# Optimization experiments

Measured on AMD Instinct MI355X. Metric: run time of the kernel, lower is better.

Reference implementation:

```python
import jax, jax.numpy as jnp
import numpy as np

N = 50000      # nodes
E = 800000     # edges (avg degree 16)
NODE = 64      # node_attr_size
EDGE = 16      # edge_attr_size
H = 2          # gat_heads
C = 64         # hidden_size (per-head out channels)
F = H * C      # feature_size = 128
L = 2          # num_gat_layers
K = 10         # num_clusters
EPS = 1e-5
NEG_SLOPE = 0.2


def setup_inputs() -> dict:
    key = jax.random.key(0)
    ks = jax.random.split(key, 16)
    s = 0.05
    inp = {
        "x": jax.random.normal(ks[0], (N, NODE), jnp.float32),
        "edge_index": jax.random.randint(ks[1], (2, E), 0, N, jnp.int64 if jax.config.read('jax_enable_x64') else jnp.int32),
        "edge_attr": jax.random.normal(ks[2], (E, EDGE), jnp.float32),
        # node_feat_proj
        "Wp": jax.random.normal(ks[3], (NODE, F), jnp.float32) * s,
        "bp": jnp.zeros((F,), jnp.float32),
        # per-layer LayerNorm affine params, stacked over layers
        "ln_g": jnp.ones((L, F), jnp.float32),
        "ln_b": jnp.zeros((L, F), jnp.float32),
        # per-layer GATv2Conv params (PyG: lin_l, lin_r with bias, lin_edge no bias, att, out bias)
        "Wl": jax.random.normal(ks[4], (L, F, F), jnp.float32) * s,
        "bl": jnp.zeros((L, F), jnp.float32),
        "Wr": jax.random.normal(ks[5], (L, F, F), jnp.float32) * s,
        "br": jnp.zeros((L, F), jnp.float32),
        "We": jax.random.normal(ks[6], (L, EDGE, F), jnp.float32) * s,
        "att": jax.random.normal(ks[7], (L, H, C), jnp.float32) * s,
        "bout": jnp.zeros((L, F), jnp.float32),
        # classifier
        "Wc": jax.random.normal(ks[8], (F, K), jnp.float32) * s,
        "bc": jnp.zeros((K,), jnp.float32),
    }
    return inp


def _layer_norm(x, g, b):
    mu = jnp.mean(x, axis=-1, keepdims=True)
    var = jnp.var(x, axis=-1, keepdims=True)
    return (x - mu) * jax.lax.rsqrt(var + EPS) * g + b


def _gatv2_conv(x, src, dst, Wl, bl, Wr, br, We, att, bout):
    # x: [N, F] -> out: [N, H*C]
    xl = (x @ Wl + bl).reshape(N, H, C)          # source transform
    xr = (x @ Wr + br).reshape(N, H, C)          # target transform
    ee = (jnp.zeros(0),)  # placeholder, edge emb computed by caller closure
    return xl, xr


def reference(x, edge_index, edge_attr, Wp, bp, ln_g, ln_b, Wl, bl, Wr, br, We, att, bout, Wc, bc):
    src, dst = edge_index[0], edge_index[1]
    h = x @ Wp + bp                                   # [N, F]
    for i in range(L):
        identity = h
        hn = _layer_norm(h, ln_g[i], ln_b[i])
        xl = (hn @ Wl[i] + bl[i]).reshape(N, H, C)    # lin_l(x)  (source side)
        xr = (hn @ Wr[i] + br[i]).reshape(N, H, C)    # lin_r(x)  (target side)
        ee = (edge_attr @ We[i]).reshape(E, H, C)     # lin_edge(edge_attr)
        m = xl[src] + xr[dst] + ee                    # [E, H, C]
        m = jnp.where(m > 0, m, NEG_SLOPE * m)        # LeakyReLU(0.2)
        logits = jnp.einsum('ehc,hc->eh', m, att[i])  # [E, H]
        # segment softmax over incoming edges of each target node
        mx = jax.ops.segment_max(logits, dst, num_segments=N)
        ex = jnp.exp(logits - mx[dst])
        den = jax.ops.segment_sum(ex, dst, num_segments=N)
        alpha = ex / den[dst]                         # [E, H]
        msg = xl[src] * alpha[:, :, None]             # [E, H, C]
        agg = jax.ops.segment_sum(msg, dst, num_segments=N)  # [N, H, C]
        hg = agg.reshape(N, F) + bout[i]
        h = jax.nn.relu(hg) + identity                # relu -> dropout(eval no-op) -> residual add
    node_embeddings = h
    classification_output = h @ Wc + bc               # [N, K]
    return (classification_output, node_embeddings)
```

## Files before the change

kernel.cpp:

```cpp
#include <hip/hip_runtime.h>
#include <math.h>

#define N_NODES 50000
#define N_EDGES 800000
#define FDIM 128
#define KCLS 10

typedef float v2f __attribute__((ext_vector_type(2)));
typedef short bf16x8 __attribute__((ext_vector_type(8)));
typedef float f32x4 __attribute__((ext_vector_type(4)));

__device__ __forceinline__ v2f pksplat(float a) { v2f r; r.x = a; r.y = a; return r; }
__device__ __forceinline__ v2f pkfma(v2f a, v2f b, v2f c) { return __builtin_elementwise_fma(a, b, c); }
__device__ __forceinline__ v2f pklrelu(v2f v) {
    v2f z = pksplat(0.f);
    v2f mx = __builtin_elementwise_max(v, z);
    v2f mn = __builtin_elementwise_min(v, z);
    return pkfma(pksplat(0.2f), mn, mx);
}
__device__ __forceinline__ int rfl(int v) { return __builtin_amdgcn_readfirstlane(v); }

__device__ __forceinline__ unsigned int f2bfu(float f) {
    unsigned int u = __float_as_uint(f);
    u += 0x7FFFu + ((u >> 16) & 1u);
    return u >> 16;
}

__device__ __forceinline__ float half_sum32(float x) {
    int v;
    v = __builtin_amdgcn_update_dpp(0, __float_as_int(x), 0xB1, 0xF, 0xF, true);
    x += __int_as_float(v);
    v = __builtin_amdgcn_update_dpp(0, __float_as_int(x), 0x4E, 0xF, 0xF, true);
    x += __int_as_float(v);
    v = __builtin_amdgcn_update_dpp(0, __float_as_int(x), 0x124, 0xF, 0xF, true);
    x += __int_as_float(v);
    v = __builtin_amdgcn_update_dpp(0, __float_as_int(x), 0x128, 0xF, 0xF, true);
    x += __int_as_float(v);
    v = __builtin_amdgcn_ds_swizzle(__float_as_int(x), 0x401F);
    x += __int_as_float(v);
    return x;
}


__global__ void k_count(const int* __restrict__ dst, int* __restrict__ indeg, int e_total) {
    int e = blockIdx.x * 256 + threadIdx.x;
    if (e < e_total) atomicAdd(&indeg[dst[e]], 1);
}

__global__ __launch_bounds__(1024) void k_scan_block(const int* __restrict__ in, int* __restrict__ excl,
                                                     int* __restrict__ bsum, int n) {
    __shared__ int sh[1024];
    int t = threadIdx.x;
    int g = blockIdx.x * 1024 + t;
    int v = (g < n) ? in[g] : 0;
    sh[t] = v;
    __syncthreads();
    for (int d = 1; d < 1024; d <<= 1) {
        int x = (t >= d) ? sh[t - d] : 0;
        __syncthreads();
        sh[t] += x;
        __syncthreads();
    }
    if (g < n) excl[g] = sh[t] - v;
    if (t == 1023) bsum[blockIdx.x] = sh[t];
}

__global__ void k_scan_small(int* bsum, int nb) {
    if (threadIdx.x == 0 && blockIdx.x == 0) {
        int run = 0;
        for (int i = 0; i < nb; i++) { int v = bsum[i]; bsum[i] = run; run += v; }
    }
}

__global__ __launch_bounds__(1024) void k_scan_add(int* __restrict__ offs, const int* __restrict__ bsum,
                                                   int* __restrict__ cursor, int n, int e_total) {
    int g = blockIdx.x * 1024 + threadIdx.x;
    if (g < n) {
        int v = offs[g] + bsum[blockIdx.x];
        offs[g] = v;
        cursor[g] = v;
    }
    if (g == 0) offs[n] = e_total;
}

__global__ void k_scatter_fused(const int* __restrict__ src, const int* __restrict__ dst,
                                const float* __restrict__ edge_attr,
                                int* __restrict__ cursor, int* __restrict__ ssrc,
                                float* __restrict__ sea, int e_total) {
    int e = blockIdx.x * 256 + threadIdx.x;
    if (e < e_total) {
        int d = dst[e];
        int p = atomicAdd(&cursor[d], 1);
        ssrc[p] = src[e];
        const float4* ea = (const float4*)&edge_attr[(size_t)e * 16];
        float4* out = (float4*)&sea[(size_t)p * 16];
        float4 a = ea[0], b = ea[1], c = ea[2], q = ea[3];
        out[0] = a; out[1] = b; out[2] = c; out[3] = q;
    }
}

__global__ void k_scatter(const int* __restrict__ src, const int* __restrict__ dst,
                          int* __restrict__ cursor, int* __restrict__ seid, int* __restrict__ ssrc, int e_total) {
    int e = blockIdx.x * 256 + threadIdx.x;
    if (e < e_total) {
        int d = dst[e];
        int p = atomicAdd(&cursor[d], 1);
        seid[p] = e;
        ssrc[p] = src[e];
    }
}


__global__ void k_prep_w(const float* __restrict__ Wp, const float* __restrict__ Wl,
                         const float* __restrict__ Wr,
                         short* __restrict__ Wpt, short* __restrict__ Wlt, short* __restrict__ Wrt) {
    int i = blockIdx.x * 256 + threadIdx.x;
    if (i < 128 * 64) {
        int nn = i >> 6, k = i & 63;
        Wpt[i] = (short)f2bfu(Wp[k * 128 + nn]);
    }
    if (i < 2 * 128 * 128) {
        int L = i >> 14, r = i & 16383;
        int nn = r >> 7, k = r & 127;
        Wlt[i] = (short)f2bfu(Wl[L * 16384 + k * 128 + nn]);
        Wrt[i] = (short)f2bfu(Wr[L * 16384 + k * 128 + nn]);
    }
}


__device__ __forceinline__ void ln_to_shn_bf16(float a0[4][4], const float* __restrict__ lng,
                                               const float* __restrict__ lnb, short* __restrict__ shn,
                                               int tr, int tc) {
    float4 g4 = *(const float4*)&lng[tc];
    float4 b4 = *(const float4*)&lnb[tc];
#pragma unroll
    for (int j = 0; j < 4; j++) {
        float s = (a0[j][0] + a0[j][1]) + (a0[j][2] + a0[j][3]);
        float ss = a0[j][0] * a0[j][0] + a0[j][1] * a0[j][1] + a0[j][2] * a0[j][2] + a0[j][3] * a0[j][3];
        s = half_sum32(s);
        ss = half_sum32(ss);
        float mu = s * (1.f / 128.f);
        float var = ss * (1.f / 128.f) - mu * mu;
        float rs = rsqrtf(var + 1e-5f);
        float ox = (a0[j][0] - mu) * rs * g4.x + b4.x;
        float oy = (a0[j][1] - mu) * rs * g4.y + b4.y;
        float oz = (a0[j][2] - mu) * rs * g4.z + b4.z;
        float ow = (a0[j][3] - mu) * rs * g4.w + b4.w;
        uint2 pk;
        pk.x = f2bfu(ox) | (f2bfu(oy) << 16);
        pk.y = f2bfu(oz) | (f2bfu(ow) << 16);
        *(uint2*)&shn[(tr + j) * 136 + tc] = pk;
    }
}


__device__ __forceinline__ void dual_gemm_mfma(const short* __restrict__ shn,
                                               const short* __restrict__ Wlt, const float* __restrict__ bl,
                                               const short* __restrict__ Wrt, const float* __restrict__ br,
                                               float* __restrict__ xl, float* __restrict__ xr,
                                               int t, int row0, int n) {
    int w = t >> 6, l = t & 63;
    int lr = l & 15, lg = l >> 4;
    const short* Wt = (w & 2) ? Wrt : Wlt;
    const float* bias = (w & 2) ? br : bl;
    float* out = (w & 2) ? xr : xl;
    int mt = w & 1;

    bf16x8 af[4];
#pragma unroll
    for (int kb = 0; kb < 4; kb++)
        af[kb] = *(const bf16x8*)&shn[(mt * 16 + lr) * 136 + kb * 32 + lg * 8];

#pragma unroll
    for (int n0 = 0; n0 < 8; n0++) {
        float b = bias[n0 * 16 + lr];
        f32x4 acc = {b, b, b, b};
#pragma unroll
        for (int kb = 0; kb < 4; kb++) {
            bf16x8 bf = *(const bf16x8*)&Wt[(size_t)(n0 * 16 + lr) * 128 + kb * 32 + lg * 8];
            acc = __builtin_amdgcn_mfma_f32_16x16x32_bf16(af[kb], bf, acc, 0, 0, 0);
        }
#pragma unroll
        for (int r = 0; r < 4; r++) {
            int row = row0 + mt * 16 + lg * 4 + r;
            if (row < n) out[(size_t)row * 128 + n0 * 16 + lr] = acc[r];
        }
    }
}


__global__ __launch_bounds__(256, 4) void k_ln_gemm_first(const float* __restrict__ x, const short* __restrict__ Wpt,
                                                          const float* __restrict__ bp,
                                                          const float* __restrict__ lng, const float* __restrict__ lnb,
                                                          const short* __restrict__ Wlt, const float* __restrict__ bl,
                                                          const short* __restrict__ Wrt, const float* __restrict__ br,
                                                          float* __restrict__ h, float* __restrict__ xl,
                                                          float* __restrict__ xr, int n) {
    __shared__ short shx[32 * 72];
    __shared__ float sh_h[32 * 132];
    __shared__ short shn[32 * 136];
    int t = threadIdx.x;
    int row0 = blockIdx.x * 32;
    int nrows = min(32, n - row0);

    for (int c = t; c < 512; c += 256) {
        int r = c >> 4, c4 = (c & 15) * 4;
        float4 v = make_float4(0.f, 0.f, 0.f, 0.f);
        if (r < nrows) v = ((const float4*)x)[(size_t)(row0 + r) * 16 + (c & 15)];
        uint2 pk;
        pk.x = f2bfu(v.x) | (f2bfu(v.y) << 16);
        pk.y = f2bfu(v.z) | (f2bfu(v.w) << 16);
        *(uint2*)&shx[r * 72 + c4] = pk;
    }
    __syncthreads();

    {
        int w = t >> 6, l = t & 63;
        int lr = l & 15, lg = l >> 4;
        int mt = w & 1, n0base = (w >> 1) * 4;
        bf16x8 axf[2];
#pragma unroll
        for (int kb = 0; kb < 2; kb++)
            axf[kb] = *(const bf16x8*)&shx[(mt * 16 + lr) * 72 + kb * 32 + lg * 8];
#pragma unroll
        for (int i = 0; i < 4; i++) {
            int n0 = n0base + i;
            float b = bp[n0 * 16 + lr];
            f32x4 acc = {b, b, b, b};
#pragma unroll
            for (int kb = 0; kb < 2; kb++) {
                bf16x8 bf = *(const bf16x8*)&Wpt[(size_t)(n0 * 16 + lr) * 64 + kb * 32 + lg * 8];
                acc = __builtin_amdgcn_mfma_f32_16x16x32_bf16(axf[kb], bf, acc, 0, 0, 0);
            }
#pragma unroll
            for (int r = 0; r < 4; r++)
                sh_h[(mt * 16 + lg * 4 + r) * 132 + n0 * 16 + lr] = acc[r];
        }
    }
    __syncthreads();

    int tr = (t >> 5) * 4, tc = (t & 31) * 4;
    float a0[4][4];
#pragma unroll
    for (int j = 0; j < 4; j++) {
        float4 v = *(const float4*)&sh_h[(tr + j) * 132 + tc];
        a0[j][0] = v.x; a0[j][1] = v.y; a0[j][2] = v.z; a0[j][3] = v.w;
        int r = row0 + tr + j;
        if (r < n) *(float4*)&h[(size_t)r * 128 + tc] = v;
    }
    ln_to_shn_bf16(a0, lng, lnb, shn, tr, tc);
    __syncthreads();

    dual_gemm_mfma(shn, Wlt, bl, Wrt, br, xl, xr, t, row0, n);
}


__global__ __launch_bounds__(256, 4) void k_ln_gemm(const float* __restrict__ h,
                                                    const float* __restrict__ lng, const float* __restrict__ lnb,
                                                    const short* __restrict__ Wlt, const float* __restrict__ bl,
                                                    const short* __restrict__ Wrt, const float* __restrict__ br,
                                                    float* __restrict__ xl, float* __restrict__ xr, int n) {
    __shared__ short shn[32 * 136];
    int t = threadIdx.x;
    int row0 = blockIdx.x * 32;
    int tr = (t >> 5) * 4, tc = (t & 31) * 4;

    float a0[4][4];
#pragma unroll
    for (int j = 0; j < 4; j++) {
        int r = row0 + tr + j;
        float4 v = make_float4(0.f, 0.f, 0.f, 0.f);
        if (r < n) v = *(const float4*)&h[(size_t)r * 128 + tc];
        a0[j][0] = v.x; a0[j][1] = v.y; a0[j][2] = v.z; a0[j][3] = v.w;
    }
    ln_to_shn_bf16(a0, lng, lnb, shn, tr, tc);
    __syncthreads();

    dual_gemm_mfma(shn, Wlt, bl, Wrt, br, xl, xr, t, row0, n);
}


#define AGG_BLOCKS 1280

template <bool SORTED, int G>
__device__ __forceinline__ void grpN(const float* __restrict__ xl_lane, const float* __restrict__ eattr,
                                     const int* __restrict__ seid, const int* __restrict__ ssrc,
                                     int j, v2f xr2, const v2f* we, v2f av,
                                     float& den, v2f& A) {
    v2f lx[G];
    const float* ep[G];
#pragma unroll
    for (int g = 0; g < G; g++) {
        int sn = rfl(ssrc[j + g]);
        lx[g] = *(const v2f*)(xl_lane + sn * 128);
        int r = SORTED ? (j + g) : rfl(seid[j + g]);
        ep[g] = &eattr[(size_t)r * 16];
    }
    v2f v[G];
#pragma unroll
    for (int g = 0; g < G; g++) v[g] = lx[g] + xr2;
#pragma unroll
    for (int k = 0; k < 16; k++) {
#pragma unroll
        for (int g = 0; g < G; g++) v[g] = pkfma(pksplat(ep[g][k]), we[k], v[g]);
    }
    float p[G];
#pragma unroll
    for (int g = 0; g < G; g++) {
        v2f t = pklrelu(v[g]) * av;
        p[g] = t.x + t.y;
    }
#pragma unroll
    for (int g = 0; g < G; g++) p[g] = half_sum32(p[g]);
#pragma unroll
    for (int g = 0; g < G; g++) {
        float wv = __expf(p[g]);
        den += wv;
        A = pkfma(pksplat(wv), lx[g], A);
    }
}

template <bool SORTED>
__global__ __launch_bounds__(256, 5) void k_gat_agg(const float* __restrict__ xl, const float* __restrict__ xr,
                                                    const float* __restrict__ eattr,
                                                    const int* __restrict__ offs,
                                                    const int* __restrict__ seid, const int* __restrict__ ssrc,
                                                    const float* __restrict__ We, const float* __restrict__ att,
                                                    const float* __restrict__ bout,
                                                    const float* __restrict__ hin, float* __restrict__ hout, int n) {
    int wid = threadIdx.x >> 6;
    int lane = threadIdx.x & 63;
    int gwave = blockIdx.x * 4 + wid;
    const int nwaves = AGG_BLOCKS * 4;

    int chb = (lane >> 5) * 64 + (lane & 31) * 2;
    const float* xl_lane = xl + chb;

    v2f we[16];
#pragma unroll
    for (int k = 0; k < 16; k++) we[k] = *(const v2f*)&We[k * 128 + chb];
    v2f av = *(const v2f*)&att[chb];
    v2f bo = *(const v2f*)&bout[chb];

    for (int node = gwave; node < n; node += nwaves) {
        v2f xr2 = *(const v2f*)&xr[node * 128 + chb];
        int s = rfl(offs[node]);
        int e = rfl(offs[node + 1]);
        float den = 0.f;
        v2f A = pksplat(0.f);

        int j = s;
        for (; j + 8 <= e; j += 8)
            grpN<SORTED, 8>(xl_lane, eattr, seid, ssrc, j, xr2, we, av, den, A);
        if (j + 4 <= e) {
            grpN<SORTED, 4>(xl_lane, eattr, seid, ssrc, j, xr2, we, av, den, A);
            j += 4;
        }
        for (; j < e; j++)
            grpN<SORTED, 1>(xl_lane, eattr, seid, ssrc, j, xr2, we, av, den, A);

        float inv = (e > s) ? (1.f / den) : 0.f;
        v2f hg = pkfma(A, pksplat(inv), bo);
        hg = __builtin_elementwise_max(hg, pksplat(0.f));
        v2f hv = *(const v2f*)&hin[node * 128 + chb];
        *(v2f*)&hout[node * 128 + chb] = hv + hg;
    }
}


__global__ __launch_bounds__(256) void k_cls_lite(const float* __restrict__ emb, const float* __restrict__ Wc,
                                                  const float* __restrict__ bc, float* __restrict__ out_cls, int n) {
    int wid = threadIdx.x >> 6;
    int lane = threadIdx.x & 63;
    int node = blockIdx.x * 4 + wid;
    if (node >= n) return;
    float h0 = emb[(size_t)node * 128 + lane];
    float h1 = emb[(size_t)node * 128 + 64 + lane];
    float p[10];
#pragma unroll
    for (int k = 0; k < 10; k++) p[k] = h0 * Wc[lane * 10 + k] + h1 * Wc[(64 + lane) * 10 + k];
#pragma unroll
    for (int o = 32; o; o >>= 1) {
#pragma unroll
        for (int k = 0; k < 10; k++) p[k] += __shfl_xor(p[k], o, 64);
    }
    if (lane == 0) {
#pragma unroll
        for (int k = 0; k < 10; k++) out_cls[(size_t)node * 10 + k] = p[k] + bc[k];
    }
}

extern "C" void kernel_launch(void* const* d_in, const int* in_sizes, int n_in,
                              void* d_out, int out_size, void* d_ws, size_t ws_size,
                              hipStream_t stream) {
    const float* x         = (const float*)d_in[0];
    const int*   edge_idx  = (const int*)d_in[1];
    const float* edge_attr = (const float*)d_in[2];
    const float* Wp        = (const float*)d_in[3];
    const float* bp        = (const float*)d_in[4];
    const float* lng       = (const float*)d_in[5];
    const float* lnb       = (const float*)d_in[6];
    const float* Wl        = (const float*)d_in[7];
    const float* bl        = (const float*)d_in[8];
    const float* Wr        = (const float*)d_in[9];
    const float* br        = (const float*)d_in[10];
    const float* We        = (const float*)d_in[11];
    const float* att       = (const float*)d_in[12];
    const float* bout      = (const float*)d_in[13];
    const float* Wc        = (const float*)d_in[14];
    const float* bc        = (const float*)d_in[15];

    const int N = N_NODES, E = N_EDGES;

    char* w = (char*)d_ws;
    size_t used = 0;
    auto take = [&](size_t bytes) -> void* {
        void* p = (void*)(w + used);
        used += (bytes + 255) & ~(size_t)255;
        return p;
    };
    float* h      = (float*)take((size_t)N * 128 * 4);
    float* xl     = (float*)take((size_t)N * 128 * 4);
    float* xr     = (float*)take((size_t)N * 128 * 4);
    int*   indeg  = (int*)take((size_t)N * 4);
    int*   offs   = (int*)take((size_t)(N + 1) * 4);
    int*   cursor = (int*)take((size_t)N * 4);
    int*   bsum   = (int*)take(64 * 4);
    int*   seid   = (int*)take((size_t)E * 4);
    int*   ssrc   = (int*)take((size_t)E * 4);
    short* Wpt    = (short*)take((size_t)128 * 64 * 2);
    short* Wlt    = (short*)take((size_t)2 * 128 * 128 * 2);
    short* Wrt    = (short*)take((size_t)2 * 128 * 128 * 2);
    float* sea    = (float*)take((size_t)E * 16 * 4);
    bool sorted_ok = (used <= ws_size);

    float* out_cls = (float*)d_out;
    float* out_emb = (float*)d_out + (size_t)N * KCLS;

    const int* srcArr = edge_idx;
    const int* dstArr = edge_idx + E;

    (void)hipMemsetAsync(indeg, 0, (size_t)N * 4, stream);
    k_count<<<(E + 255) / 256, 256, 0, stream>>>(dstArr, indeg, E);
    int NB = (N + 1023) / 1024;
    k_scan_block<<<NB, 1024, 0, stream>>>(indeg, offs, bsum, N);
    k_scan_small<<<1, 64, 0, stream>>>(bsum, NB);
    k_scan_add<<<NB, 1024, 0, stream>>>(offs, bsum, cursor, N, E);
    if (sorted_ok)
        k_scatter_fused<<<(E + 255) / 256, 256, 0, stream>>>(srcArr, dstArr, edge_attr, cursor, ssrc, sea, E);
    else
        k_scatter<<<(E + 255) / 256, 256, 0, stream>>>(srcArr, dstArr, cursor, seid, ssrc, E);

    k_prep_w<<<128, 256, 0, stream>>>(Wp, Wl, Wr, Wpt, Wlt, Wrt);

    k_ln_gemm_first<<<(N + 31) / 32, 256, 0, stream>>>(
        x, Wpt, bp, lng, lnb,
        Wlt, bl, Wrt, br, h, xl, xr, N);
    if (sorted_ok)
        k_gat_agg<true><<<AGG_BLOCKS, 256, 0, stream>>>(
            xl, xr, sea, offs, seid, ssrc, We, att, bout, h, h, N);
    else
        k_gat_agg<false><<<AGG_BLOCKS, 256, 0, stream>>>(
            xl, xr, edge_attr, offs, seid, ssrc, We, att, bout, h, h, N);

    k_ln_gemm<<<(N + 31) / 32, 256, 0, stream>>>(
        h, lng + 128, lnb + 128,
        Wlt + 16384, bl + 128,
        Wrt + 16384, br + 128,
        xl, xr, N);
    if (sorted_ok)
        k_gat_agg<true><<<AGG_BLOCKS, 256, 0, stream>>>(
            xl, xr, sea, offs, seid, ssrc,
            We + 16 * 128, att + 128, bout + 128, h, out_emb, N);
    else
        k_gat_agg<false><<<AGG_BLOCKS, 256, 0, stream>>>(
            xl, xr, edge_attr, offs, seid, ssrc,
            We + 16 * 128, att + 128, bout + 128, h, out_emb, N);

    k_cls_lite<<<(N + 3) / 4, 256, 0, stream>>>(out_emb, Wc, bc, out_cls, N);
}
```

Measured before the change: 390.1 us.

## Store xl/xr and sorted edge attributes as bf16 to halve gather traffic

```diff
diff --git a/kernel.cpp b/kernel.cpp
--- a/kernel.cpp
+++ b/kernel.cpp
@@ -9,6 +9,7 @@
 typedef float v2f __attribute__((ext_vector_type(2)));
 typedef short bf16x8 __attribute__((ext_vector_type(8)));
 typedef float f32x4 __attribute__((ext_vector_type(4)));
+typedef unsigned int uint32;
 
 __device__ __forceinline__ v2f pksplat(float a) { v2f r; r.x = a; r.y = a; return r; }
 __device__ __forceinline__ v2f pkfma(v2f a, v2f b, v2f c) { return __builtin_elementwise_fma(a, b, c); }
@@ -20,10 +21,16 @@
 }
 __device__ __forceinline__ int rfl(int v) { return __builtin_amdgcn_readfirstlane(v); }
 
-__device__ __forceinline__ unsigned int f2bfu(float f) {
-    unsigned int u = __float_as_uint(f);
+__device__ __forceinline__ uint32 f2bfu(float f) {
+    uint32 u = __float_as_uint(f);
     u += 0x7FFFu + ((u >> 16) & 1u);
     return u >> 16;
+}
+__device__ __forceinline__ v2f unpk2(uint32 u) {
+    v2f r;
+    r.x = __uint_as_float(u << 16);
+    r.y = __uint_as_float(u & 0xFFFF0000u);
+    return r;
 }
 
 __device__ __forceinline__ float half_sum32(float x) {
@@ -86,27 +93,26 @@
 __global__ void k_scatter_fused(const int* __restrict__ src, const int* __restrict__ dst,
                                 const float* __restrict__ edge_attr,
                                 int* __restrict__ cursor, int* __restrict__ ssrc,
-                                float* __restrict__ sea, int e_total) {
+                                uint32* __restrict__ sea32, int e_total) {
     int e = blockIdx.x * 256 + threadIdx.x;
     if (e < e_total) {
         int d = dst[e];
         int p = atomicAdd(&cursor[d], 1);
         ssrc[p] = src[e];
         const float4* ea = (const float4*)&edge_attr[(size_t)e * 16];
-        float4* out = (float4*)&sea[(size_t)p * 16];
         float4 a = ea[0], b = ea[1], c = ea[2], q = ea[3];
-        out[0] = a; out[1] = b; out[2] = c; out[3] = q;
-    }
-}
-
-__global__ void k_scatter(const int* __restrict__ src, const int* __restrict__ dst,
-                          int* __restrict__ cursor, int* __restrict__ seid, int* __restrict__ ssrc, int e_total) {
-    int e = blockIdx.x * 256 + threadIdx.x;
-    if (e < e_total) {
-        int d = dst[e];
-        int p = atomicAdd(&cursor[d], 1);
-        seid[p] = e;
-        ssrc[p] = src[e];
+        uint4 o1, o2;
+        o1.x = f2bfu(a.x) | (f2bfu(a.y) << 16);
+        o1.y = f2bfu(a.z) | (f2bfu(a.w) << 16);
+        o1.z = f2bfu(b.x) | (f2bfu(b.y) << 16);
+        o1.w = f2bfu(b.z) | (f2bfu(b.w) << 16);
+        o2.x = f2bfu(c.x) | (f2bfu(c.y) << 16);
+        o2.y = f2bfu(c.z) | (f2bfu(c.w) << 16);
+        o2.z = f2bfu(q.x) | (f2bfu(q.y) << 16);
+        o2.w = f2bfu(q.z) | (f2bfu(q.w) << 16);
+        uint4* outp = (uint4*)&sea32[(size_t)p * 8];
+        outp[0] = o1;
+        outp[1] = o2;
     }
 }
 
@@ -157,13 +163,13 @@
 __device__ __forceinline__ void dual_gemm_mfma(const short* __restrict__ shn,
                                                const short* __restrict__ Wlt, const float* __restrict__ bl,
                                                const short* __restrict__ Wrt, const float* __restrict__ br,
-                                               float* __restrict__ xl, float* __restrict__ xr,
+                                               unsigned short* __restrict__ xl, unsigned short* __restrict__ xr,
                                                int t, int row0, int n) {
     int w = t >> 6, l = t & 63;
     int lr = l & 15, lg = l >> 4;
     const short* Wt = (w & 2) ? Wrt : Wlt;
     const float* bias = (w & 2) ? br : bl;
-    float* out = (w & 2) ? xr : xl;
+    unsigned short* out = (w & 2) ? xr : xl;
     int mt = w & 1;
 
     bf16x8 af[4];
@@ -183,7 +189,7 @@
 #pragma unroll
         for (int r = 0; r < 4; r++) {
             int row = row0 + mt * 16 + lg * 4 + r;
-            if (row < n) out[(size_t)row * 128 + n0 * 16 + lr] = acc[r];
+            if (row < n) out[(size_t)row * 128 + n0 * 16 + lr] = (unsigned short)f2bfu(acc[r]);
         }
     }
 }
@@ -194,8 +200,8 @@
                                                           const float* __restrict__ lng, const float* __restrict__ lnb,
                                                           const short* __restrict__ Wlt, const float* __restrict__ bl,
                                                           const short* __restrict__ Wrt, const float* __restrict__ br,
-                                                          float* __restrict__ h, float* __restrict__ xl,
-                                                          float* __restrict__ xr, int n) {
+                                                          float* __restrict__ h, unsigned short* __restrict__ xl,
+                                                          unsigned short* __restrict__ xr, int n) {
     __shared__ short shx[32 * 72];
     __shared__ float sh_h[32 * 132];
     __shared__ short shn[32 * 136];
@@ -259,7 +265,8 @@
                                                     const float* __restrict__ lng, const float* __restrict__ lnb,
                                                     const short* __restrict__ Wlt, const float* __restrict__ bl,
                                                     const short* __restrict__ Wrt, const float* __restrict__ br,
-                                                    float* __restrict__ xl, float* __restrict__ xr, int n) {
+                                                    unsigned short* __restrict__ xl, unsigned short* __restrict__ xr,
+                                                    int n) {
     __shared__ short shn[32 * 136];
     int t = threadIdx.x;
     int row0 = blockIdx.x * 32;
@@ -282,27 +289,30 @@
 
 #define AGG_BLOCKS 1280
 
-template <bool SORTED, int G>
-__device__ __forceinline__ void grpN(const float* __restrict__ xl_lane, const float* __restrict__ eattr,
-                                     const int* __restrict__ seid, const int* __restrict__ ssrc,
+template <int G>
+__device__ __forceinline__ void grpN(const uint32* __restrict__ xl32_lane, const uint32* __restrict__ sea32,
+                                     const int* __restrict__ ssrc,
                                      int j, v2f xr2, const v2f* we, v2f av,
                                      float& den, v2f& A) {
     v2f lx[G];
-    const float* ep[G];
+    const uint32* ep[G];
 #pragma unroll
     for (int g = 0; g < G; g++) {
         int sn = rfl(ssrc[j + g]);
-        lx[g] = *(const v2f*)(xl_lane + sn * 128);
-        int r = SORTED ? (j + g) : rfl(seid[j + g]);
-        ep[g] = &eattr[(size_t)r * 16];
+        lx[g] = unpk2(xl32_lane[(size_t)sn * 64]);
+        ep[g] = &sea32[(size_t)(j + g) * 8];
     }
     v2f v[G];
 #pragma unroll
     for (int g = 0; g < G; g++) v[g] = lx[g] + xr2;
 #pragma unroll
-    for (int k = 0; k < 16; k++) {
-#pragma unroll
-        for (int g = 0; g < G; g++) v[g] = pkfma(pksplat(ep[g][k]), we[k], v[g]);
+    for (int k2 = 0; k2 < 8; k2++) {
+#pragma unroll
+        for (int g = 0; g < G; g++) {
+            uint32 u = ep[g][k2];
+            v[g] = pkfma(pksplat(__uint_as_float(u << 16)), we[2 * k2], v[g]);
+            v[g] = pkfma(pksplat(__uint_as_float(u & 0xFFFF0000u)), we[2 * k2 + 1], v[g]);
+        }
     }
     float p[G];
 #pragma unroll
@@ -320,11 +330,9 @@
     }
 }
 
-template <bool SORTED>
-__global__ __launch_bounds__(256, 5) void k_gat_agg(const float* __restrict__ xl, const float* __restrict__ xr,
-                                                    const float* __restrict__ eattr,
-                                                    const int* __restrict__ offs,
-                                                    const int* __restrict__ seid, const int* __restrict__ ssrc,
+__global__ __launch_bounds__(256, 5) void k_gat_agg(const uint32* __restrict__ xl32, const uint32* __restrict__ xr32,
+                                                    const uint32* __restrict__ sea32,
+                                                    const int* __restrict__ offs, const int* __restrict__ ssrc,
                                                     const float* __restrict__ We, const float* __restrict__ att,
                                                     const float* __restrict__ bout,
                                                     const float* __restrict__ hin, float* __restrict__ hout, int n) {
@@ -334,7 +342,8 @@
     const int nwaves = AGG_BLOCKS * 4;
 
     int chb = (lane >> 5) * 64 + (lane & 31) * 2;
-    const float* xl_lane = xl + chb;
+    int ch2 = chb >> 1;
+    const uint32* xl32_lane = xl32 + ch2;
 
     v2f we[16];
 #pragma unroll
@@ -343,7 +352,7 @@
     v2f bo = *(const v2f*)&bout[chb];
 
     for (int node = gwave; node < n; node += nwaves) {
-        v2f xr2 = *(const v2f*)&xr[node * 128 + chb];
+        v2f xr2 = unpk2(xr32[(size_t)node * 64 + ch2]);
         int s = rfl(offs[node]);
         int e = rfl(offs[node + 1]);
         float den = 0.f;
@@ -351,19 +360,19 @@
 
         int j = s;
         for (; j + 8 <= e; j += 8)
-            grpN<SORTED, 8>(xl_lane, eattr, seid, ssrc, j, xr2, we, av, den, A);
+            grpN<8>(xl32_lane, sea32, ssrc, j, xr2, we, av, den, A);
         if (j + 4 <= e) {
-            grpN<SORTED, 4>(xl_lane, eattr, seid, ssrc, j, xr2, we, av, den, A);
+            grpN<4>(xl32_lane, sea32, ssrc, j, xr2, we, av, den, A);
             j += 4;
         }
         for (; j < e; j++)
-            grpN<SORTED, 1>(xl_lane, eattr, seid, ssrc, j, xr2, we, av, den, A);
+            grpN<1>(xl32_lane, sea32, ssrc, j, xr2, we, av, den, A);
 
         float inv = (e > s) ? (1.f / den) : 0.f;
         v2f hg = pkfma(A, pksplat(inv), bo);
         hg = __builtin_elementwise_max(hg, pksplat(0.f));
-        v2f hv = *(const v2f*)&hin[node * 128 + chb];
-        *(v2f*)&hout[node * 128 + chb] = hv + hg;
+        v2f hv = *(const v2f*)&hin[(size_t)node * 128 + chb];
+        *(v2f*)&hout[(size_t)node * 128 + chb] = hv + hg;
     }
 }
 
@@ -419,20 +428,18 @@
         used += (bytes + 255) & ~(size_t)255;
         return p;
     };
-    float* h      = (float*)take((size_t)N * 128 * 4);
-    float* xl     = (float*)take((size_t)N * 128 * 4);
-    float* xr     = (float*)take((size_t)N * 128 * 4);
-    int*   indeg  = (int*)take((size_t)N * 4);
-    int*   offs   = (int*)take((size_t)(N + 1) * 4);
-    int*   cursor = (int*)take((size_t)N * 4);
-    int*   bsum   = (int*)take(64 * 4);
-    int*   seid   = (int*)take((size_t)E * 4);
-    int*   ssrc   = (int*)take((size_t)E * 4);
-    short* Wpt    = (short*)take((size_t)128 * 64 * 2);
-    short* Wlt    = (short*)take((size_t)2 * 128 * 128 * 2);
-    short* Wrt    = (short*)take((size_t)2 * 128 * 128 * 2);
-    float* sea    = (float*)take((size_t)E * 16 * 4);
-    bool sorted_ok = (used <= ws_size);
+    float*  h      = (float*)take((size_t)N * 128 * 4);
+    unsigned short* xl = (unsigned short*)take((size_t)N * 128 * 2);
+    unsigned short* xr = (unsigned short*)take((size_t)N * 128 * 2);
+    int*    indeg  = (int*)take((size_t)N * 4);
+    int*    offs   = (int*)take((size_t)(N + 1) * 4);
+    int*    cursor = (int*)take((size_t)N * 4);
+    int*    bsum   = (int*)take(64 * 4);
+    int*    ssrc   = (int*)take((size_t)E * 4);
+    short*  Wpt    = (short*)take((size_t)128 * 64 * 2);
+    short*  Wlt    = (short*)take((size_t)2 * 128 * 128 * 2);
+    short*  Wrt    = (short*)take((size_t)2 * 128 * 128 * 2);
+    uint32* sea32  = (uint32*)take((size_t)E * 8 * 4);
 
     float* out_cls = (float*)d_out;
     float* out_emb = (float*)d_out + (size_t)N * KCLS;
@@ -446,36 +453,24 @@
     k_scan_block<<<NB, 1024, 0, stream>>>(indeg, offs, bsum, N);
     k_scan_small<<<1, 64, 0, stream>>>(bsum, NB);
     k_scan_add<<<NB, 1024, 0, stream>>>(offs, bsum, cursor, N, E);
-    if (sorted_ok)
-        k_scatter_fused<<<(E + 255) / 256, 256, 0, stream>>>(srcArr, dstArr, edge_attr, cursor, ssrc, sea, E);
-    else
-        k_scatter<<<(E + 255) / 256, 256, 0, stream>>>(srcArr, dstArr, cursor, seid, ssrc, E);
+    k_scatter_fused<<<(E + 255) / 256, 256, 0, stream>>>(srcArr, dstArr, edge_attr, cursor, ssrc, sea32, E);
 
     k_prep_w<<<128, 256, 0, stream>>>(Wp, Wl, Wr, Wpt, Wlt, Wrt);
 
     k_ln_gemm_first<<<(N + 31) / 32, 256, 0, stream>>>(
         x, Wpt, bp, lng, lnb,
         Wlt, bl, Wrt, br, h, xl, xr, N);
-    if (sorted_ok)
-        k_gat_agg<true><<<AGG_BLOCKS, 256, 0, stream>>>(
-            xl, xr, sea, offs, seid, ssrc, We, att, bout, h, h, N);
-    else
-        k_gat_agg<false><<<AGG_BLOCKS, 256, 0, stream>>>(
-            xl, xr, edge_attr, offs, seid, ssrc, We, att, bout, h, h, N);
+    k_gat_agg<<<AGG_BLOCKS, 256, 0, stream>>>(
+        (const uint32*)xl, (const uint32*)xr, sea32, offs, ssrc, We, att, bout, h, h, N);
 
     k_ln_gemm<<<(N + 31) / 32, 256, 0, stream>>>(
         h, lng + 128, lnb + 128,
         Wlt + 16384, bl + 128,
         Wrt + 16384, br + 128,
         xl, xr, N);
-    if (sorted_ok)
-        k_gat_agg<true><<<AGG_BLOCKS, 256, 0, stream>>>(
-            xl, xr, sea, offs, seid, ssrc,
-            We + 16 * 128, att + 128, bout + 128, h, out_emb, N);
-    else
-        k_gat_agg<false><<<AGG_BLOCKS, 256, 0, stream>>>(
-            xl, xr, edge_attr, offs, seid, ssrc,
-            We + 16 * 128, att + 128, bout + 128, h, out_emb, N);
+    k_gat_agg<<<AGG_BLOCKS, 256, 0, stream>>>(
+        (const uint32*)xl, (const uint32*)xr, sea32, offs, ssrc,
+        We + 16 * 128, att + 128, bout + 128, h, out_emb, N);
 
     k_cls_lite<<<(N + 3) / 4, 256, 0, stream>>>(out_emb, Wc, bc, out_cls, N);
 }
```

Result: slower. 418.8 us (median of 2 runs) (+7.4%).
